# Kernel tuning notes

Hardware: AMD Instinct MI355X
Metric: run time of the kernel (lower is better)

The kernel has to match this reference:

```python
import jax, jax.numpy as jnp
import numpy as np

N_NODES = 50000
N_EDGES = 400000
N_GRAPHS = 512
NF = 64      # node_features
EF = 32      # edge_features (RBF bins)
AIF = 92     # atom_input_features
FC = 128     # fc_features
L = 3        # conv layers
EPS = 1e-5   # BatchNorm eps


def _bn(x, gamma, beta):
    # BatchNorm1d, training-mode statistics over the batch (edge/node) dim
    m = x.mean(0)
    v = x.var(0)  # biased variance, matches torch normalization
    return (x - m) * jax.lax.rsqrt(v + EPS) * gamma + beta


def _rbf(d):
    # RBFExpansion(vmin=0, vmax=8, bins=EF): gamma = 1/mean(diff(centers))
    centers = jnp.linspace(0.0, 8.0, EF)
    gamma = 1.0 / (centers[1] - centers[0])
    return jnp.exp(-gamma * (d[:, None] - centers) ** 2)  # [E, EF]


def setup_inputs() -> dict:
    key = jax.random.key(0)
    ks = jax.random.split(key, 12)
    s = 0.05
    IN = 2 * NF + EF
    return {
        "atom_features": jax.random.normal(ks[0], (N_NODES, AIF), dtype=jnp.float32),
        "bondlength": jax.random.uniform(ks[1], (N_EDGES,), dtype=jnp.float32) * 8.0,
        "src": jax.random.randint(ks[2], (N_EDGES,), 0, N_NODES),
        "dst": jax.random.randint(ks[3], (N_EDGES,), 0, N_NODES),
        "graph_ids": jnp.sort(jax.random.randint(ks[4], (N_NODES,), 0, N_GRAPHS)),
        "W_emb": jax.random.normal(ks[5], (AIF, NF), dtype=jnp.float32) * s,
        "b_emb": jnp.zeros((NF,), jnp.float32),
        "Wi": jax.random.normal(ks[6], (L, IN, NF), dtype=jnp.float32) * s,
        "bi": jnp.zeros((L, NF), jnp.float32),
        "gi": jnp.ones((L, NF), jnp.float32),
        "bti": jnp.zeros((L, NF), jnp.float32),
        "Wu": jax.random.normal(ks[7], (L, IN, NF), dtype=jnp.float32) * s,
        "bu": jnp.zeros((L, NF), jnp.float32),
        "gu": jnp.ones((L, NF), jnp.float32),
        "btu": jnp.zeros((L, NF), jnp.float32),
        "g_bn": jnp.ones((L, NF), jnp.float32),
        "b_bn": jnp.zeros((L, NF), jnp.float32),
        "W_fc": jax.random.normal(ks[8], (NF, FC), dtype=jnp.float32) * s,
        "b_fc": jnp.zeros((FC,), jnp.float32),
        "W_out": jax.random.normal(ks[9], (FC, 1), dtype=jnp.float32) * s,
        "b_out": jnp.zeros((1,), jnp.float32),
    }


def reference(atom_features, bondlength, src, dst, graph_ids,
              W_emb, b_emb, Wi, bi, gi, bti, Wu, bu, gu, btu,
              g_bn, b_bn, W_fc, b_fc, W_out, b_out):
    e = _rbf(bondlength)                       # [E, EF]
    h = atom_features @ W_emb + b_emb          # [N, NF]
    for l in range(L):
        # gather + concat: [E, 2*NF + EF]
        z = jnp.concatenate([h[src], h[dst], e], axis=1)
        gate = jax.nn.sigmoid(_bn(z @ Wi[l] + bi[l], gi[l], bti[l]))
        upd = jax.nn.softplus(_bn(z @ Wu[l] + bu[l], gu[l], btu[l]))
        msg = gate * upd                       # [E, NF]
        agg = jax.ops.segment_sum(msg, dst, num_segments=N_NODES)
        h = jax.nn.softplus(h + _bn(agg, g_bn[l], b_bn[l]))
    # AvgPooling over nodes per graph
    counts = jax.ops.segment_sum(jnp.ones((N_NODES, 1), h.dtype), graph_ids,
                                 num_segments=N_GRAPHS)
    pooled = jax.ops.segment_sum(h, graph_ids, num_segments=N_GRAPHS)
    pooled = pooled / jnp.maximum(counts, 1.0)  # [G, NF]
    f = jax.nn.softplus(pooled)
    f = jax.nn.softplus(f @ W_fc + b_fc)
    f = jax.nn.softplus(f)
    out = f @ W_out + b_out                    # [G, 1]
    return jnp.squeeze(out)                    # [G]
```

## Files before the change

### kernel.cpp

```cpp
#include <hip/hip_runtime.h>
#include <math.h>

#define N_NODES 50000
#define N_EDGES 400000
#define N_GRAPHS 512
#define TBL 2048
#define EPSBN 1e-5f

__device__ __forceinline__ float softplusf(float x) {
  return fmaxf(x, 0.0f) + log1pf(expf(-fabsf(x)));
}
__device__ __forceinline__ float sigmoidf(float x) {
  return 1.0f / (1.0f + expf(-x));
}

__global__ void k_emb(const float* __restrict__ atom,
                      const float* __restrict__ Wemb,
                      const float* __restrict__ bemb,
                      float* __restrict__ h) {
  __shared__ float sW[92 * 64];
  for (int i = threadIdx.x; i < 92 * 64; i += blockDim.x) sW[i] = Wemb[i];
  __syncthreads();
  const int wave = threadIdx.x >> 6, lane = threadIdx.x & 63;
  const int wpb = blockDim.x >> 6;
  const int nw = wpb * gridDim.x;
  const float bb = bemb[lane];
  for (int n = blockIdx.x * wpb + wave; n < N_NODES; n += nw) {
    const float* ar = atom + (size_t)n * 92;
    float acc = bb;
#pragma unroll
    for (int k = 0; k < 92; ++k) acc = fmaf(ar[k], sW[k * 64 + lane], acc);
    h[(size_t)n * 64 + lane] = acc;
  }
}

__global__ void k_pq(const float* __restrict__ h,
                     const float* __restrict__ Wi_l,
                     const float* __restrict__ Wu_l,
                     float* __restrict__ PQ) {
  __shared__ float sW[2][64 * 64];
  const int wave = threadIdx.x >> 6, lane = threadIdx.x & 63;
  const int wpb = blockDim.x >> 6;
  const int nw = wpb * gridDim.x;
  for (int ph = 0; ph < 2; ++ph) {
    const float* W = ph ? Wu_l : Wi_l;
    __syncthreads();
    for (int i = threadIdx.x; i < 64 * 64; i += blockDim.x) {
      sW[0][i] = W[i];
      sW[1][i] = W[64 * 64 + i];
    }
    __syncthreads();
    float* P = PQ + (size_t)(2 * ph) * N_NODES * 64;
    float* Q = PQ + (size_t)(2 * ph + 1) * N_NODES * 64;
    for (int n = blockIdx.x * wpb + wave; n < N_NODES; n += nw) {
      float hv = h[(size_t)n * 64 + lane];
      float a0 = 0.f, a1 = 0.f;
#pragma unroll
      for (int k = 0; k < 64; ++k) {
        float hk = __shfl(hv, k);
        a0 = fmaf(hk, sW[0][k * 64 + lane], a0);
        a1 = fmaf(hk, sW[1][k * 64 + lane], a1);
      }
      P[(size_t)n * 64 + lane] = a0;
      Q[(size_t)n * 64 + lane] = a1;
    }
  }
}

__global__ void k_tbl(const float* __restrict__ Wi_l,
                      const float* __restrict__ Wu_l,
                      float* __restrict__ tbl) {
  const int wave = threadIdx.x >> 6, lane = threadIdx.x & 63;
  const int t = blockIdx.x * (blockDim.x >> 6) + wave;
  if (t >= TBL) return;
  const float d = 8.0f * (float)t / (float)(TBL - 1);
  float gi_ = 0.f, gu_ = 0.f;
#pragma unroll
  for (int k = 0; k < 32; ++k) {
    float c = 8.0f * (float)k / 31.0f;
    float dd = d - c;
    float r = expf(-3.875f * dd * dd);
    gi_ = fmaf(r, Wi_l[(128 + k) * 64 + lane], gi_);
    gu_ = fmaf(r, Wu_l[(128 + k) * 64 + lane], gu_);
  }
  tbl[(size_t)t * 64 + lane] = gi_;
  tbl[(size_t)TBL * 64 + (size_t)t * 64 + lane] = gu_;
}

__device__ __forceinline__ void edge_pre(int e, int lane,
                                         const int* __restrict__ src,
                                         const int* __restrict__ dst,
                                         const float* __restrict__ bond,
                                         const float* __restrict__ PQ,
                                         const float* __restrict__ tbl,
                                         float& yg, float& yu, int& dnode) {
  const int s = src[e];
  const int d2 = dst[e];
  const float d = bond[e];
  float f = d * ((float)(TBL - 1) / 8.0f);
  f = fminf(fmaxf(f, 0.0f), (float)(TBL - 1));
  int i0 = (int)f;
  if (i0 > TBL - 2) i0 = TBL - 2;
  const float fr = f - (float)i0;
  const float* tg = tbl + (size_t)i0 * 64 + lane;
  const float* tu = tg + (size_t)TBL * 64;
  const float rg = fmaf(fr, tg[64] - tg[0], tg[0]);
  const float ru = fmaf(fr, tu[64] - tu[0], tu[0]);
  yg = PQ[(size_t)s * 64 + lane] + PQ[((size_t)N_NODES + d2) * 64 + lane] + rg;
  yu = PQ[((size_t)2 * N_NODES + s) * 64 + lane] +
       PQ[((size_t)3 * N_NODES + d2) * 64 + lane] + ru;
  dnode = d2;
}

__global__ void k_edge_stats(const int* __restrict__ src,
                             const int* __restrict__ dst,
                             const float* __restrict__ bond,
                             const float* __restrict__ PQ,
                             const float* __restrict__ tbl,
                             float* __restrict__ stats) {
  const int wave = threadIdx.x >> 6, lane = threadIdx.x & 63;
  const int wpb = blockDim.x >> 6;
  const int nw = wpb * gridDim.x;
  float sg = 0.f, qg = 0.f, su = 0.f, qu = 0.f;
  for (int e = blockIdx.x * wpb + wave; e < N_EDGES; e += nw) {
    float yg, yu; int dn;
    edge_pre(e, lane, src, dst, bond, PQ, tbl, yg, yu, dn);
    sg += yg; qg = fmaf(yg, yg, qg);
    su += yu; qu = fmaf(yu, yu, qu);
  }
  __shared__ float red[4][4][64];
  red[0][wave][lane] = sg;
  red[1][wave][lane] = qg;
  red[2][wave][lane] = su;
  red[3][wave][lane] = qu;
  __syncthreads();
  float v = red[wave][0][lane] + red[wave][1][lane] + red[wave][2][lane] + red[wave][3][lane];
  atomicAdd(&stats[wave * 64 + lane], v);
}

__global__ void k_fin_gu(const float* __restrict__ stats,
                         const float* __restrict__ gi_l, const float* __restrict__ bti_l,
                         const float* __restrict__ gu_l, const float* __restrict__ btu_l,
                         float* __restrict__ coefs) {
  const int j = threadIdx.x;
  const float invE = 1.0f / (float)N_EDGES;
  float m = stats[j] * invE;
  float v = stats[64 + j] * invE - m * m;
  float a = gi_l[j] * rsqrtf(v + EPSBN);
  coefs[j] = a;
  coefs[64 + j] = fmaf(-m, a, bti_l[j]);
  m = stats[128 + j] * invE;
  v = stats[192 + j] * invE - m * m;
  a = gu_l[j] * rsqrtf(v + EPSBN);
  coefs[128 + j] = a;
  coefs[192 + j] = fmaf(-m, a, btu_l[j]);
}

__global__ void k_edge_apply(const int* __restrict__ src,
                             const int* __restrict__ dst,
                             const float* __restrict__ bond,
                             const float* __restrict__ PQ,
                             const float* __restrict__ tbl,
                             const float* __restrict__ coefs,
                             float* __restrict__ agg) {
  const int wave = threadIdx.x >> 6, lane = threadIdx.x & 63;
  const int wpb = blockDim.x >> 6;
  const int nw = wpb * gridDim.x;
  const float ag = coefs[lane], bg = coefs[64 + lane];
  const float au = coefs[128 + lane], bu = coefs[192 + lane];
  for (int e = blockIdx.x * wpb + wave; e < N_EDGES; e += nw) {
    float yg, yu; int dn;
    edge_pre(e, lane, src, dst, bond, PQ, tbl, yg, yu, dn);
    const float gate = sigmoidf(fmaf(ag, yg, bg));
    const float upd = softplusf(fmaf(au, yu, bu));
    atomicAdd(&agg[(size_t)dn * 64 + lane], gate * upd);
  }
}

__global__ void k_agg_stats(const float* __restrict__ agg, float* __restrict__ stats) {
  const int wave = threadIdx.x >> 6, lane = threadIdx.x & 63;
  const int wpb = blockDim.x >> 6;
  const int nw = wpb * gridDim.x;
  float s = 0.f, q = 0.f;
  for (int n = blockIdx.x * wpb + wave; n < N_NODES; n += nw) {
    float v = agg[(size_t)n * 64 + lane];
    s += v; q = fmaf(v, v, q);
  }
  __shared__ float red[2][4][64];
  red[0][wave][lane] = s;
  red[1][wave][lane] = q;
  __syncthreads();
  if (wave < 2) {
    float v = red[wave][0][lane] + red[wave][1][lane] + red[wave][2][lane] + red[wave][3][lane];
    atomicAdd(&stats[256 + wave * 64 + lane], v);
  }
}

__global__ void k_fin_agg(const float* __restrict__ stats,
                          const float* __restrict__ gbn_l, const float* __restrict__ bbn_l,
                          float* __restrict__ coefs) {
  const int j = threadIdx.x;
  const float invN = 1.0f / (float)N_NODES;
  float m = stats[256 + j] * invN;
  float v = stats[320 + j] * invN - m * m;
  float a = gbn_l[j] * rsqrtf(v + EPSBN);
  coefs[256 + j] = a;
  coefs[320 + j] = fmaf(-m, a, bbn_l[j]);
}

__global__ void k_hupd(float* __restrict__ h, const float* __restrict__ agg,
                       const float* __restrict__ coefs) {
  const int stride = blockDim.x * gridDim.x;
  for (int i = blockIdx.x * blockDim.x + threadIdx.x; i < N_NODES * 64; i += stride) {
    const int j = i & 63;
    float x = h[i] + fmaf(coefs[256 + j], agg[i], coefs[320 + j]);
    h[i] = softplusf(x);
  }
}

__global__ void k_pool(const float* __restrict__ h, const int* __restrict__ gid,
                       float* __restrict__ pooled, float* __restrict__ counts) {
  const int wave = threadIdx.x >> 6, lane = threadIdx.x & 63;
  const int wpb = blockDim.x >> 6;
  const int nw = wpb * gridDim.x;
  for (int n = blockIdx.x * wpb + wave; n < N_NODES; n += nw) {
    const int g = gid[n];
    atomicAdd(&pooled[(size_t)g * 64 + lane], h[(size_t)n * 64 + lane]);
    if (lane == 0) atomicAdd(&counts[g], 1.0f);
  }
}

__global__ void k_final(const float* __restrict__ pooled, const float* __restrict__ counts,
                        const float* __restrict__ Wfc, const float* __restrict__ bfc,
                        const float* __restrict__ Wout, const float* __restrict__ bout,
                        float* __restrict__ out) {
  __shared__ float f1[64];
  __shared__ float red[128];
  const int g = blockIdx.x, t = threadIdx.x;
  if (t < 64) {
    const float c = fmaxf(counts[g], 1.0f);
    f1[t] = softplusf(pooled[(size_t)g * 64 + t] / c);
  }
  __syncthreads();
  float acc = bfc[t];
#pragma unroll
  for (int k = 0; k < 64; ++k) acc = fmaf(f1[k], Wfc[k * 128 + t], acc);
  red[t] = softplusf(softplusf(acc)) * Wout[t];
  __syncthreads();
  for (int s2 = 64; s2 > 0; s2 >>= 1) {
    if (t < s2) red[t] += red[t + s2];
    __syncthreads();
  }
  if (t == 0) out[g] = red[0] + bout[0];
}

extern "C" void kernel_launch(void* const* d_in, const int* in_sizes, int n_in,
                              void* d_out, int out_size, void* d_ws, size_t ws_size,
                              hipStream_t stream) {
  const float* atom = (const float*)d_in[0];
  const float* bond = (const float*)d_in[1];
  const int* src = (const int*)d_in[2];
  const int* dst = (const int*)d_in[3];
  const int* gid = (const int*)d_in[4];
  const float* Wemb = (const float*)d_in[5];
  const float* bemb = (const float*)d_in[6];
  const float* Wi = (const float*)d_in[7];
  const float* gi = (const float*)d_in[9];
  const float* bti = (const float*)d_in[10];
  const float* Wu = (const float*)d_in[11];
  const float* gub = (const float*)d_in[13];
  const float* btu = (const float*)d_in[14];
  const float* gbn = (const float*)d_in[15];
  const float* bbn = (const float*)d_in[16];
  const float* Wfc = (const float*)d_in[17];
  const float* bfc = (const float*)d_in[18];
  const float* Wout = (const float*)d_in[19];
  const float* bout = (const float*)d_in[20];

  float* h = (float*)d_ws;
  float* PQ = h + (size_t)N_NODES * 64;
  float* agg = PQ + (size_t)4 * N_NODES * 64;
  float* tbl = agg + (size_t)N_NODES * 64;
  float* stats = tbl + (size_t)2 * TBL * 64;
  float* coefs = stats + 384;
  float* pooled = coefs + 384;
  float* counts = pooled + (size_t)N_GRAPHS * 64;

  k_emb<<<512, 256, 0, stream>>>(atom, Wemb, bemb, h);
  for (int l = 0; l < 3; ++l) {
    const float* Wi_l = Wi + (size_t)l * 160 * 64;
    const float* Wu_l = Wu + (size_t)l * 160 * 64;
    hipMemsetAsync(stats, 0, 384 * sizeof(float), stream);
    hipMemsetAsync(agg, 0, (size_t)N_NODES * 64 * sizeof(float), stream);
    k_pq<<<512, 256, 0, stream>>>(h, Wi_l, Wu_l, PQ);
    k_tbl<<<TBL / 4, 256, 0, stream>>>(Wi_l, Wu_l, tbl);
    k_edge_stats<<<1024, 256, 0, stream>>>(src, dst, bond, PQ, tbl, stats);
    k_fin_gu<<<1, 64, 0, stream>>>(stats, gi + l * 64, bti + l * 64,
                                   gub + l * 64, btu + l * 64, coefs);
    k_edge_apply<<<1024, 256, 0, stream>>>(src, dst, bond, PQ, tbl, coefs, agg);
    k_agg_stats<<<512, 256, 0, stream>>>(agg, stats);
    k_fin_agg<<<1, 64, 0, stream>>>(stats, gbn + l * 64, bbn + l * 64, coefs);
    k_hupd<<<1024, 256, 0, stream>>>(h, agg, coefs);
  }
  hipMemsetAsync(pooled, 0, (size_t)(N_GRAPHS * 64 + N_GRAPHS) * sizeof(float), stream);
  k_pool<<<512, 256, 0, stream>>>(h, gid, pooled, counts);
  k_final<<<N_GRAPHS, 128, 0, stream>>>(pooled, counts, Wfc, bfc, Wout, bout,
                                        (float*)d_out);
}
```

Measured before the change: 1.810 ms.

## Interleave gate/update projections per node and register-tile node GEMMs

Source and destination projections for the gate and update paths are now stored interleaved as [N,128] (PA for src, PB for dst), and the RBF table is interleaved likewise. Each edge then reads two contiguous 512-byte rows instead of four scattered 256-byte rows, which is meant to improve gather locality. The embedding and projection kernels are rewritten as 32-node tiles staged in shared memory, with register blocking and float4 weight reads. Edge kernel grids are doubled. The larger shared-memory footprint of k_pq (about 72 KB) may limit occupancy.

```diff
diff --git a/kernel.cpp b/kernel.cpp
--- a/kernel.cpp
+++ b/kernel.cpp
@@ -13,57 +13,113 @@
 __device__ __forceinline__ float sigmoidf(float x) {
   return 1.0f / (1.0f + expf(-x));
 }
+__device__ __forceinline__ void fma4(float4& acc, float s, const float4& w) {
+  acc.x = fmaf(s, w.x, acc.x);
+  acc.y = fmaf(s, w.y, acc.y);
+  acc.z = fmaf(s, w.z, acc.z);
+  acc.w = fmaf(s, w.w, acc.w);
+}
 
 __global__ void k_emb(const float* __restrict__ atom,
                       const float* __restrict__ Wemb,
                       const float* __restrict__ bemb,
                       float* __restrict__ h) {
   __shared__ float sW[92 * 64];
-  for (int i = threadIdx.x; i < 92 * 64; i += blockDim.x) sW[i] = Wemb[i];
-  __syncthreads();
-  const int wave = threadIdx.x >> 6, lane = threadIdx.x & 63;
-  const int wpb = blockDim.x >> 6;
-  const int nw = wpb * gridDim.x;
-  const float bb = bemb[lane];
-  for (int n = blockIdx.x * wpb + wave; n < N_NODES; n += nw) {
-    const float* ar = atom + (size_t)n * 92;
-    float acc = bb;
-#pragma unroll
-    for (int k = 0; k < 92; ++k) acc = fmaf(ar[k], sW[k * 64 + lane], acc);
-    h[(size_t)n * 64 + lane] = acc;
+  __shared__ float sA[32 * 92];
+  const int tid = threadIdx.x;
+  for (int i = tid; i < 92 * 64; i += 256) sW[i] = Wemb[i];
+
+  const int t0 = blockIdx.x * 32;
+  const int nt = min(32, N_NODES - t0);
+  {
+    const float* srcp = atom + (size_t)t0 * 92;
+    const int tot = nt * 92;
+    for (int i = tid; i < tot; i += 256) sA[i] = srcp[i];
+  }
+  __syncthreads();
+
+  const int col = tid & 63;
+  const int ng = tid >> 6;
+  const float bb = bemb[col];
+  float acc[8];
+#pragma unroll
+  for (int i = 0; i < 8; ++i) acc[i] = bb;
+
+  for (int kc = 0; kc < 92; kc += 4) {
+    const float w0 = sW[(kc + 0) * 64 + col];
+    const float w1 = sW[(kc + 1) * 64 + col];
+    const float w2 = sW[(kc + 2) * 64 + col];
+    const float w3 = sW[(kc + 3) * 64 + col];
+#pragma unroll
+    for (int i = 0; i < 8; ++i) {
+      const float4 a = *(const float4*)&sA[(ng * 8 + i) * 92 + kc];
+      acc[i] = fmaf(a.x, w0, acc[i]);
+      acc[i] = fmaf(a.y, w1, acc[i]);
+      acc[i] = fmaf(a.z, w2, acc[i]);
+      acc[i] = fmaf(a.w, w3, acc[i]);
+    }
+  }
+#pragma unroll
+  for (int i = 0; i < 8; ++i) {
+    const int n = t0 + ng * 8 + i;
+    if (n < N_NODES) h[(size_t)n * 64 + col] = acc[i];
   }
 }
 
 __global__ void k_pq(const float* __restrict__ h,
                      const float* __restrict__ Wi_l,
                      const float* __restrict__ Wu_l,
-                     float* __restrict__ PQ) {
-  __shared__ float sW[2][64 * 64];
-  const int wave = threadIdx.x >> 6, lane = threadIdx.x & 63;
-  const int wpb = blockDim.x >> 6;
-  const int nw = wpb * gridDim.x;
-  for (int ph = 0; ph < 2; ++ph) {
-    const float* W = ph ? Wu_l : Wi_l;
-    __syncthreads();
-    for (int i = threadIdx.x; i < 64 * 64; i += blockDim.x) {
-      sW[0][i] = W[i];
-      sW[1][i] = W[64 * 64 + i];
+                     float* __restrict__ PA,
+                     float* __restrict__ PB) {
+  __shared__ float sWA[64 * 128];
+  __shared__ float sWB[64 * 128];
+  __shared__ float sH[32 * 64];
+  const int tid = threadIdx.x;
+
+  for (int i = tid; i < 64 * 64; i += 256) {
+    const int k = i >> 6, c = i & 63;
+    sWA[k * 128 + c]      = Wi_l[k * 64 + c];
+    sWA[k * 128 + 64 + c] = Wu_l[k * 64 + c];
+    sWB[k * 128 + c]      = Wi_l[(64 + k) * 64 + c];
+    sWB[k * 128 + 64 + c] = Wu_l[(64 + k) * 64 + c];
+  }
+  const int t0 = blockIdx.x * 32;
+  const int nt = min(32, N_NODES - t0);
+  {
+    const float4* srcp = (const float4*)(h + (size_t)t0 * 64);
+    const int tot4 = nt * 16;
+    float4* dstp = (float4*)sH;
+    for (int i = tid; i < tot4; i += 256) dstp[i] = srcp[i];
+  }
+  __syncthreads();
+
+  const int wave = tid >> 6, lane = tid & 63;
+  const float* wcol = (lane < 32) ? (sWA + 4 * lane) : (sWB + 4 * (lane - 32));
+  const int jj = (lane < 32) ? 4 * lane : 4 * (lane - 32);
+  float* OUTb = (lane < 32) ? PA : PB;
+
+  float4 acc[8];
+#pragma unroll
+  for (int i = 0; i < 8; ++i) acc[i] = make_float4(0.f, 0.f, 0.f, 0.f);
+
+  for (int kc = 0; kc < 64; kc += 4) {
+    const float4 w0 = *(const float4*)(wcol + (kc + 0) * 128);
+    const float4 w1 = *(const float4*)(wcol + (kc + 1) * 128);
+    const float4 w2 = *(const float4*)(wcol + (kc + 2) * 128);
+    const float4 w3 = *(const float4*)(wcol + (kc + 3) * 128);
+#pragma unroll
+    for (int i = 0; i < 8; ++i) {
+      const float4 a = *(const float4*)&sH[(wave * 8 + i) * 64 + kc];
+      fma4(acc[i], a.x, w0);
+      fma4(acc[i], a.y, w1);
+      fma4(acc[i], a.z, w2);
+      fma4(acc[i], a.w, w3);
     }
-    __syncthreads();
-    float* P = PQ + (size_t)(2 * ph) * N_NODES * 64;
-    float* Q = PQ + (size_t)(2 * ph + 1) * N_NODES * 64;
-    for (int n = blockIdx.x * wpb + wave; n < N_NODES; n += nw) {
-      float hv = h[(size_t)n * 64 + lane];
-      float a0 = 0.f, a1 = 0.f;
-#pragma unroll
-      for (int k = 0; k < 64; ++k) {
-        float hk = __shfl(hv, k);
-        a0 = fmaf(hk, sW[0][k * 64 + lane], a0);
-        a1 = fmaf(hk, sW[1][k * 64 + lane], a1);
-      }
-      P[(size_t)n * 64 + lane] = a0;
-      Q[(size_t)n * 64 + lane] = a1;
-    }
+  }
+#pragma unroll
+  for (int i = 0; i < 8; ++i) {
+    const int n = t0 + wave * 8 + i;
+    if (n < N_NODES) *(float4*)&OUTb[(size_t)n * 128 + jj] = acc[i];
   }
 }
 
@@ -77,21 +133,22 @@
   float gi_ = 0.f, gu_ = 0.f;
 #pragma unroll
   for (int k = 0; k < 32; ++k) {
-    float c = 8.0f * (float)k / 31.0f;
-    float dd = d - c;
-    float r = expf(-3.875f * dd * dd);
+    const float c = 8.0f * (float)k / 31.0f;
+    const float dd = d - c;
+    const float r = expf(-3.875f * dd * dd);
     gi_ = fmaf(r, Wi_l[(128 + k) * 64 + lane], gi_);
     gu_ = fmaf(r, Wu_l[(128 + k) * 64 + lane], gu_);
   }
-  tbl[(size_t)t * 64 + lane] = gi_;
-  tbl[(size_t)TBL * 64 + (size_t)t * 64 + lane] = gu_;
+  tbl[(size_t)t * 128 + lane] = gi_;
+  tbl[(size_t)t * 128 + 64 + lane] = gu_;
 }
 
 __device__ __forceinline__ void edge_pre(int e, int lane,
                                          const int* __restrict__ src,
                                          const int* __restrict__ dst,
                                          const float* __restrict__ bond,
-                                         const float* __restrict__ PQ,
+                                         const float* __restrict__ PA,
+                                         const float* __restrict__ PB,
                                          const float* __restrict__ tbl,
                                          float& yg, float& yu, int& dnode) {
   const int s = src[e];
@@ -102,20 +159,21 @@
   int i0 = (int)f;
   if (i0 > TBL - 2) i0 = TBL - 2;
   const float fr = f - (float)i0;
-  const float* tg = tbl + (size_t)i0 * 64 + lane;
-  const float* tu = tg + (size_t)TBL * 64;
-  const float rg = fmaf(fr, tg[64] - tg[0], tg[0]);
-  const float ru = fmaf(fr, tu[64] - tu[0], tu[0]);
-  yg = PQ[(size_t)s * 64 + lane] + PQ[((size_t)N_NODES + d2) * 64 + lane] + rg;
-  yu = PQ[((size_t)2 * N_NODES + s) * 64 + lane] +
-       PQ[((size_t)3 * N_NODES + d2) * 64 + lane] + ru;
+  const float* ta = tbl + (size_t)i0 * 128 + lane;
+  const float rg = fmaf(fr, ta[128] - ta[0], ta[0]);
+  const float ru = fmaf(fr, ta[192] - ta[64], ta[64]);
+  const float* pa = PA + (size_t)s * 128 + lane;
+  const float* pb = PB + (size_t)d2 * 128 + lane;
+  yg = pa[0] + pb[0] + rg;
+  yu = pa[64] + pb[64] + ru;
   dnode = d2;
 }
 
 __global__ void k_edge_stats(const int* __restrict__ src,
                              const int* __restrict__ dst,
                              const float* __restrict__ bond,
-                             const float* __restrict__ PQ,
+                             const float* __restrict__ PA,
+                             const float* __restrict__ PB,
                              const float* __restrict__ tbl,
                              float* __restrict__ stats) {
   const int wave = threadIdx.x >> 6, lane = threadIdx.x & 63;
@@ -124,7 +182,7 @@
   float sg = 0.f, qg = 0.f, su = 0.f, qu = 0.f;
   for (int e = blockIdx.x * wpb + wave; e < N_EDGES; e += nw) {
     float yg, yu; int dn;
-    edge_pre(e, lane, src, dst, bond, PQ, tbl, yg, yu, dn);
+    edge_pre(e, lane, src, dst, bond, PA, PB, tbl, yg, yu, dn);
     sg += yg; qg = fmaf(yg, yg, qg);
     su += yu; qu = fmaf(yu, yu, qu);
   }
@@ -134,7 +192,8 @@
   red[2][wave][lane] = su;
   red[3][wave][lane] = qu;
   __syncthreads();
-  float v = red[wave][0][lane] + red[wave][1][lane] + red[wave][2][lane] + red[wave][3][lane];
+  const float v = red[wave][0][lane] + red[wave][1][lane] +
+                  red[wave][2][lane] + red[wave][3][lane];
   atomicAdd(&stats[wave * 64 + lane], v);
 }
 
@@ -159,7 +218,8 @@
 __global__ void k_edge_apply(const int* __restrict__ src,
                              const int* __restrict__ dst,
                              const float* __restrict__ bond,
-                             const float* __restrict__ PQ,
+                             const float* __restrict__ PA,
+                             const float* __restrict__ PB,
                              const float* __restrict__ tbl,
                              const float* __restrict__ coefs,
                              float* __restrict__ agg) {
@@ -170,7 +230,7 @@
   const float au = coefs[128 + lane], bu = coefs[192 + lane];
   for (int e = blockIdx.x * wpb + wave; e < N_EDGES; e += nw) {
     float yg, yu; int dn;
-    edge_pre(e, lane, src, dst, bond, PQ, tbl, yg, yu, dn);
+    edge_pre(e, lane, src, dst, bond, PA, PB, tbl, yg, yu, dn);
     const float gate = sigmoidf(fmaf(ag, yg, bg));
     const float upd = softplusf(fmaf(au, yu, bu));
     atomicAdd(&agg[(size_t)dn * 64 + lane], gate * upd);
@@ -183,7 +243,7 @@
   const int nw = wpb * gridDim.x;
   float s = 0.f, q = 0.f;
   for (int n = blockIdx.x * wpb + wave; n < N_NODES; n += nw) {
-    float v = agg[(size_t)n * 64 + lane];
+    const float v = agg[(size_t)n * 64 + lane];
     s += v; q = fmaf(v, v, q);
   }
   __shared__ float red[2][4][64];
@@ -191,7 +251,8 @@
   red[1][wave][lane] = q;
   __syncthreads();
   if (wave < 2) {
-    float v = red[wave][0][lane] + red[wave][1][lane] + red[wave][2][lane] + red[wave][3][lane];
+    const float v = red[wave][0][lane] + red[wave][1][lane] +
+                    red[wave][2][lane] + red[wave][3][lane];
     atomicAdd(&stats[256 + wave * 64 + lane], v);
   }
 }
@@ -201,9 +262,9 @@
                           float* __restrict__ coefs) {
   const int j = threadIdx.x;
   const float invN = 1.0f / (float)N_NODES;
-  float m = stats[256 + j] * invN;
-  float v = stats[320 + j] * invN - m * m;
-  float a = gbn_l[j] * rsqrtf(v + EPSBN);
+  const float m = stats[256 + j] * invN;
+  const float v = stats[320 + j] * invN - m * m;
+  const float a = gbn_l[j] * rsqrtf(v + EPSBN);
   coefs[256 + j] = a;
   coefs[320 + j] = fmaf(-m, a, bbn_l[j]);
 }
@@ -213,7 +274,7 @@
   const int stride = blockDim.x * gridDim.x;
   for (int i = blockIdx.x * blockDim.x + threadIdx.x; i < N_NODES * 64; i += stride) {
     const int j = i & 63;
-    float x = h[i] + fmaf(coefs[256 + j], agg[i], coefs[320 + j]);
+    const float x = h[i] + fmaf(coefs[256 + j], agg[i], coefs[320 + j]);
     h[i] = softplusf(x);
   }
 }
@@ -278,31 +339,34 @@
   const float* bout = (const float*)d_in[20];
 
   float* h = (float*)d_ws;
-  float* PQ = h + (size_t)N_NODES * 64;
-  float* agg = PQ + (size_t)4 * N_NODES * 64;
+  float* PA = h + (size_t)N_NODES * 64;
+  float* PB = PA + (size_t)N_NODES * 128;
+  float* agg = PB + (size_t)N_NODES * 128;
   float* tbl = agg + (size_t)N_NODES * 64;
-  float* stats = tbl + (size_t)2 * TBL * 64;
+  float* stats = tbl + (size_t)TBL * 128;
   float* coefs = stats + 384;
   float* pooled = coefs + 384;
   float* counts = pooled + (size_t)N_GRAPHS * 64;
 
-  k_emb<<<512, 256, 0, stream>>>(atom, Wemb, bemb, h);
+  const int ntiles = (N_NODES + 31) / 32;
+
+  k_emb<<<ntiles, 256, 0, stream>>>(atom, Wemb, bemb, h);
   for (int l = 0; l < 3; ++l) {
     const float* Wi_l = Wi + (size_t)l * 160 * 64;
     const float* Wu_l = Wu + (size_t)l * 160 * 64;
-    hipMemsetAsync(stats, 0, 384 * sizeof(float), stream);
-    hipMemsetAsync(agg, 0, (size_t)N_NODES * 64 * sizeof(float), stream);
-    k_pq<<<512, 256, 0, stream>>>(h, Wi_l, Wu_l, PQ);
+    (void)hipMemsetAsync(stats, 0, 384 * sizeof(float), stream);
+    (void)hipMemsetAsync(agg, 0, (size_t)N_NODES * 64 * sizeof(float), stream);
+    k_pq<<<ntiles, 256, 0, stream>>>(h, Wi_l, Wu_l, PA, PB);
     k_tbl<<<TBL / 4, 256, 0, stream>>>(Wi_l, Wu_l, tbl);
-    k_edge_stats<<<1024, 256, 0, stream>>>(src, dst, bond, PQ, tbl, stats);
+    k_edge_stats<<<2048, 256, 0, stream>>>(src, dst, bond, PA, PB, tbl, stats);
     k_fin_gu<<<1, 64, 0, stream>>>(stats, gi + l * 64, bti + l * 64,
                                    gub + l * 64, btu + l * 64, coefs);
-    k_edge_apply<<<1024, 256, 0, stream>>>(src, dst, bond, PQ, tbl, coefs, agg);
+    k_edge_apply<<<2048, 256, 0, stream>>>(src, dst, bond, PA, PB, tbl, coefs, agg);
     k_agg_stats<<<512, 256, 0, stream>>>(agg, stats);
     k_fin_agg<<<1, 64, 0, stream>>>(stats, gbn + l * 64, bbn + l * 64, coefs);
     k_hupd<<<1024, 256, 0, stream>>>(h, agg, coefs);
   }
-  hipMemsetAsync(pooled, 0, (size_t)(N_GRAPHS * 64 + N_GRAPHS) * sizeof(float), stream);
+  (void)hipMemsetAsync(pooled, 0, (size_t)(N_GRAPHS * 64 + N_GRAPHS) * sizeof(float), stream);
   k_pool<<<512, 256, 0, stream>>>(h, gid, pooled, counts);
   k_final<<<N_GRAPHS, 128, 0, stream>>>(pooled, counts, Wfc, bfc, Wout, bout,
                                         (float*)d_out);
```

New measurement: 1.791 ms. Within noise of the previous version (-1.0%).
